# Performance work log

Hardware: AMD Instinct MI355X
Metric: run time of the kernel (lower is better)

## Reference

```python
import jax, jax.numpy as jnp
import numpy as np

NQ = 10          # qubits per register
DIM = 2 ** NQ    # 1024 amplitudes
N_CLS = 10       # canonical images (one per class)
N = 16384        # batch of samples
IMG = 28 * 28    # 784 pixels, zero-padded to DIM


def setup_inputs() -> dict:
    key = jax.random.key(0)
    k1, k2, k3 = jax.random.split(key, 3)
    z_re = jax.random.normal(k1, (N, DIM), dtype=jnp.float32)
    z_im = jax.random.normal(k2, (N, DIM), dtype=jnp.float32)
    # inputs are quantum states -> L2-normalize the complex vectors
    nrm = jnp.sqrt(jnp.sum(z_re * z_re + z_im * z_im, axis=1, keepdims=True))
    z_re = z_re / nrm
    z_im = z_im / nrm
    canon = jax.random.uniform(k3, (N_CLS, 1, 28, 28), dtype=jnp.float32)
    return {"z_re": z_re, "z_im": z_im, "canon": canon}


def reference(z_re, z_im, canon):
    # reshape_norm_padding: flatten, zero-pad to 2^nq, L2-normalize (real amplitudes)
    ref = canon.reshape(N_CLS, IMG)
    ref = jnp.pad(ref, ((0, 0), (0, DIM - IMG)))                  # [C, DIM]
    ref = ref / jnp.linalg.norm(ref, axis=1, keepdims=True)
    # Swap test: <Z_anc> = |<val|ref>|^2. ref is real, so with val = z_re + i*z_im:
    #   <val|ref> = (z_re @ ref^T) - i*(z_im @ ref^T)
    s_re = jnp.einsum('nd,cd->nc', z_re, ref)                     # [N, C]
    s_im = jnp.einsum('nd,cd->nc', z_im, ref)                     # [N, C]
    return s_re * s_re + s_im * s_im                              # [N, C] float32
```

## Files before the change

### kernel.cpp

```cpp
#include <hip/hip_runtime.h>

#define NQ    10
#define DIM   1024
#define N_CLS 10
#define NROWS 16384
#define IMG   784

#define ROWS_PER_BLK 8

__device__ __forceinline__ float wave64_sum(float x) {
#define DPP_ADD(ctrl, rmask, bmask)                                           \
  x += __int_as_float(__builtin_amdgcn_update_dpp(                            \
      0, __float_as_int(x), ctrl, rmask, bmask, true));
  DPP_ADD(0x111, 0xf, 0xf)
  DPP_ADD(0x112, 0xf, 0xf)
  DPP_ADD(0x114, 0xf, 0xe)
  DPP_ADD(0x118, 0xf, 0xc)
  DPP_ADD(0x142, 0xa, 0xf)
  DPP_ADD(0x143, 0xc, 0xf)
#undef DPP_ADD
  return x;
}

__global__ void ref_prep_kernel(const float* __restrict__ canon,
                                float* __restrict__ ref) {
  __shared__ float red[256];
  const int c = blockIdx.x;
  const int t = threadIdx.x;
  const float* src = canon + c * IMG;

  float ss = 0.f;
  for (int d = t; d < IMG; d += 256) {
    float v = src[d];
    ss += v * v;
  }
  red[t] = ss;
  __syncthreads();
  for (int s = 128; s > 0; s >>= 1) {
    if (t < s) red[t] += red[t + s];
    __syncthreads();
  }
  const float inv = 1.0f / sqrtf(red[0]);

  for (int d = t; d < DIM; d += 256) {
    ref[c * DIM + d] = (d < IMG) ? src[d] * inv : 0.f;
  }
}

__global__ __launch_bounds__(64, 2) void swaptest_kernel(
    const float* __restrict__ zre, const float* __restrict__ zim,
    const float* __restrict__ ref, float* __restrict__ out) {
  const int lane = threadIdx.x;

  float4 refv[4][N_CLS];
#pragma unroll
  for (int k = 0; k < 4; ++k) {
#pragma unroll
    for (int c = 0; c < N_CLS; ++c) {
      refv[k][c] =
          *(const float4*)(ref + c * DIM + k * 256 + lane * 4);
    }
  }

  const int row0 = blockIdx.x * ROWS_PER_BLK;

  for (int r = 0; r < ROWS_PER_BLK; ++r) {
    const int row = row0 + r;
    if (row >= NROWS) break;

    const float4* pre = (const float4*)(zre + (size_t)row * DIM);
    const float4* pim = (const float4*)(zim + (size_t)row * DIM);

    float4 zr[4], zi[4];
#pragma unroll
    for (int k = 0; k < 4; ++k) {
      zr[k] = pre[k * 64 + lane];
      zi[k] = pim[k * 64 + lane];
    }

    float are[N_CLS], aim[N_CLS];
#pragma unroll
    for (int c = 0; c < N_CLS; ++c) {
      are[c] = 0.f;
      aim[c] = 0.f;
    }

#pragma unroll
    for (int k = 0; k < 4; ++k) {
#pragma unroll
      for (int c = 0; c < N_CLS; ++c) {
        const float4 rv = refv[k][c];
        are[c] += zr[k].x * rv.x + zr[k].y * rv.y + zr[k].z * rv.z +
                  zr[k].w * rv.w;
        aim[c] += zi[k].x * rv.x + zi[k].y * rv.y + zi[k].z * rv.z +
                  zi[k].w * rv.w;
      }
    }

#pragma unroll
    for (int c = 0; c < N_CLS; ++c) {
      are[c] = wave64_sum(are[c]);
      aim[c] = wave64_sum(aim[c]);
    }

    if (lane == 63) {
#pragma unroll
      for (int c = 0; c < N_CLS; ++c) {
        out[(size_t)row * N_CLS + c] = are[c] * are[c] + aim[c] * aim[c];
      }
    }
  }
}

extern "C" void kernel_launch(void* const* d_in, const int* in_sizes, int n_in,
                              void* d_out, int out_size, void* d_ws,
                              size_t ws_size, hipStream_t stream) {
  const float* z_re = (const float*)d_in[0];
  const float* z_im = (const float*)d_in[1];
  const float* canon = (const float*)d_in[2];
  float* out = (float*)d_out;
  float* ref = (float*)d_ws;

  ref_prep_kernel<<<N_CLS, 256, 0, stream>>>(canon, ref);

  const int nblk = NROWS / ROWS_PER_BLK;
  swaptest_kernel<<<nblk, 64, 0, stream>>>(z_re, z_im, ref, out);
}
```

Baseline: 151.9 us.

## Fuse ref prep into MFMA kernel using split-bf16 matmul and skip padded tail

Drops the separate reference-normalisation kernel. Each block now normalises the canonical images and stores them in shared memory as hi/lo bf16 pairs. The dot products run on 16x16x32 bf16 MFMA with a three-term split (hi*hi, lo*hi, hi*lo) to approach fp32 accuracy. Only the first 832 columns of z are read, because the reference is zero beyond 784, which cuts the memory traffic. Register prefetch of upcoming z chunks is meant to overlap load latency, at the cost of redundant per-block reference prep and a small precision loss from the split-bf16 products.

Result: slower. 157.0 us (+3.4%).

```diff
diff --git a/kernel.cpp b/kernel.cpp
--- a/kernel.cpp
+++ b/kernel.cpp
@@ -1,12 +1,48 @@
 #include <hip/hip_runtime.h>
 
-#define NQ    10
-#define DIM   1024
-#define N_CLS 10
-#define NROWS 16384
-#define IMG   784
+#define DIM    1024
+#define N_CLS  10
+#define NROWS  16384
+#define IMG    784
 
-#define ROWS_PER_BLK 8
+#define KPAD   832
+#define KSTEP  26
+#define PF     6
+
+using f32x4  = __attribute__((ext_vector_type(4))) float;
+using bf16x8 = __attribute__((ext_vector_type(8))) short;
+typedef unsigned int u32;
+typedef unsigned short u16;
+
+union frag_cast {
+  u32 i[4];
+  bf16x8 h;
+  f32x4 f;
+};
+
+static __device__ __forceinline__ u16 bf16_rne(float f) {
+  u32 u = __float_as_uint(f);
+  return (u16)((u + 0x7fffu + ((u >> 16) & 1u)) >> 16);
+}
+
+static __device__ __forceinline__ void split8(const f32x4 v0, const f32x4 v1,
+                                              bf16x8& hi, bf16x8& lo) {
+  const float f[8] = {v0.x, v0.y, v0.z, v0.w, v1.x, v1.y, v1.z, v1.w};
+  frag_cast H, L;
+#pragma unroll
+  for (int i = 0; i < 4; ++i) {
+    const u32 a = __float_as_uint(f[2 * i]);
+    const u32 b = __float_as_uint(f[2 * i + 1]);
+    H.i[i] = (a >> 16) | (b & 0xffff0000u);
+    const float l0 = f[2 * i] - __uint_as_float(a & 0xffff0000u);
+    const float l1 = f[2 * i + 1] - __uint_as_float(b & 0xffff0000u);
+    u32 p;
+    asm("v_cvt_pk_bf16_f32 %0, %1, %2" : "=v"(p) : "v"(l0), "v"(l1));
+    L.i[i] = p;
+  }
+  hi = H.h;
+  lo = L.h;
+}
 
 __device__ __forceinline__ float wave64_sum(float x) {
 #define DPP_ADD(ctrl, rmask, bmask)                                           \
@@ -22,92 +58,94 @@
   return x;
 }
 
-__global__ void ref_prep_kernel(const float* __restrict__ canon,
-                                float* __restrict__ ref) {
-  __shared__ float red[256];
-  const int c = blockIdx.x;
+__global__ __launch_bounds__(256, 1) void swaptest_kernel(
+    const float* __restrict__ zre, const float* __restrict__ zim,
+    const float* __restrict__ canon, float* __restrict__ out) {
+  __shared__ u16 bhi[KSTEP * 4 * 16 * 8];
+  __shared__ u16 blo[KSTEP * 4 * 16 * 8];
+  __shared__ float linv[16];
+
   const int t = threadIdx.x;
-  const float* src = canon + c * IMG;
+  const int lane = t & 63;
+  const int wave = t >> 6;
 
-  float ss = 0.f;
-  for (int d = t; d < IMG; d += 256) {
-    float v = src[d];
-    ss += v * v;
+  for (int c = wave; c < N_CLS; c += 4) {
+    float ss = 0.f;
+    for (int i = lane; i < IMG; i += 64) {
+      const float v = canon[c * IMG + i];
+      ss += v * v;
+    }
+    ss = wave64_sum(ss);
+    if (lane == 63) linv[c] = 1.0f / sqrtf(ss);
   }
-  red[t] = ss;
   __syncthreads();
-  for (int s = 128; s > 0; s >>= 1) {
-    if (t < s) red[t] += red[t + s];
-    __syncthreads();
+
+  for (int idx = t; idx < KPAD * 16; idx += 256) {
+    const int k = idx >> 4;
+    const int c = idx & 15;
+    float val = 0.f;
+    if (c < N_CLS && k < IMG) val = canon[c * IMG + k] * linv[c];
+    const int s = k >> 5, g = (k >> 3) & 3, j = k & 7;
+    const int pos = ((s * 4 + g) * 16 + c) * 8 + j;
+    const u32 u = __float_as_uint(val);
+    bhi[pos] = (u16)(u >> 16);
+    blo[pos] = bf16_rne(val - __uint_as_float(u & 0xffff0000u));
   }
-  const float inv = 1.0f / sqrtf(red[0]);
+  __syncthreads();
 
-  for (int d = t; d < DIM; d += 256) {
-    ref[c * DIM + d] = (d < IMG) ? src[d] * inv : 0.f;
-  }
-}
+  const int wid = blockIdx.x * 4 + wave;
+  const int row0 = wid * 16;
+  const int l15 = lane & 15;
+  const int gr = lane >> 4;
 
-__global__ __launch_bounds__(64, 2) void swaptest_kernel(
-    const float* __restrict__ zre, const float* __restrict__ zim,
-    const float* __restrict__ ref, float* __restrict__ out) {
-  const int lane = threadIdx.x;
+  const f32x4* pre = (const f32x4*)(zre + (size_t)(row0 + l15) * DIM) + gr * 2;
+  const f32x4* pim = (const f32x4*)(zim + (size_t)(row0 + l15) * DIM) + gr * 2;
 
-  float4 refv[4][N_CLS];
+  f32x4 r0[PF], r1[PF], i0[PF], i1[PF];
 #pragma unroll
-  for (int k = 0; k < 4; ++k) {
-#pragma unroll
-    for (int c = 0; c < N_CLS; ++c) {
-      refv[k][c] =
-          *(const float4*)(ref + c * DIM + k * 256 + lane * 4);
-    }
+  for (int j = 0; j < PF; ++j) {
+    r0[j] = pre[j * 8];
+    r1[j] = pre[j * 8 + 1];
+    i0[j] = pim[j * 8];
+    i1[j] = pim[j * 8 + 1];
   }
 
-  const int row0 = blockIdx.x * ROWS_PER_BLK;
-
-  for (int r = 0; r < ROWS_PER_BLK; ++r) {
-    const int row = row0 + r;
-    if (row >= NROWS) break;
-
-    const float4* pre = (const float4*)(zre + (size_t)row * DIM);
-    const float4* pim = (const float4*)(zim + (size_t)row * DIM);
-
-    float4 zr[4], zi[4];
-#pragma unroll
-    for (int k = 0; k < 4; ++k) {
-      zr[k] = pre[k * 64 + lane];
-      zi[k] = pim[k * 64 + lane];
-    }
-
-    float are[N_CLS], aim[N_CLS];
-#pragma unroll
-    for (int c = 0; c < N_CLS; ++c) {
-      are[c] = 0.f;
-      aim[c] = 0.f;
-    }
+  f32x4 accre = {0.f, 0.f, 0.f, 0.f};
+  f32x4 accim = {0.f, 0.f, 0.f, 0.f};
 
 #pragma unroll
-    for (int k = 0; k < 4; ++k) {
+  for (int j = 0; j < KSTEP; ++j) {
+    const int b = j % PF;
+    bf16x8 arh, arl, aih, ail;
+    split8(r0[b], r1[b], arh, arl);
+    split8(i0[b], i1[b], aih, ail);
+    if (j + PF < KSTEP) {
+      r0[b] = pre[(j + PF) * 8];
+      r1[b] = pre[(j + PF) * 8 + 1];
+      i0[b] = pim[(j + PF) * 8];
+      i1[b] = pim[(j + PF) * 8 + 1];
+    }
+    frag_cast BH, BL;
+    const int be = (j * 64 + gr * 16 + l15) * 8;
+    BH.f = *(const f32x4*)&bhi[be];
+    BL.f = *(const f32x4*)&blo[be];
+
+    accre = __builtin_amdgcn_mfma_f32_16x16x32_bf16(arh, BH.h, accre, 0, 0, 0);
+    accre = __builtin_amdgcn_mfma_f32_16x16x32_bf16(arl, BH.h, accre, 0, 0, 0);
+    accre = __builtin_amdgcn_mfma_f32_16x16x32_bf16(arh, BL.h, accre, 0, 0, 0);
+    accim = __builtin_amdgcn_mfma_f32_16x16x32_bf16(aih, BH.h, accim, 0, 0, 0);
+    accim = __builtin_amdgcn_mfma_f32_16x16x32_bf16(ail, BH.h, accim, 0, 0, 0);
+    accim = __builtin_amdgcn_mfma_f32_16x16x32_bf16(aih, BL.h, accim, 0, 0, 0);
+  }
+
+  const int c = l15;
+  const int rbase = row0 + gr * 4;
+  if (c < N_CLS) {
 #pragma unroll
-      for (int c = 0; c < N_CLS; ++c) {
-        const float4 rv = refv[k][c];
-        are[c] += zr[k].x * rv.x + zr[k].y * rv.y + zr[k].z * rv.z +
-                  zr[k].w * rv.w;
-        aim[c] += zi[k].x * rv.x + zi[k].y * rv.y + zi[k].z * rv.z +
-                  zi[k].w * rv.w;
-      }
-    }
-
-#pragma unroll
-    for (int c = 0; c < N_CLS; ++c) {
-      are[c] = wave64_sum(are[c]);
-      aim[c] = wave64_sum(aim[c]);
-    }
-
-    if (lane == 63) {
-#pragma unroll
-      for (int c = 0; c < N_CLS; ++c) {
-        out[(size_t)row * N_CLS + c] = are[c] * are[c] + aim[c] * aim[c];
-      }
+    for (int i = 0; i < 4; ++i) {
+      const float sre = accre[i];
+      const float sim = accim[i];
+      out[(size_t)(rbase + i) * N_CLS + c] = sre * sre + sim * sim;
     }
   }
 }
@@ -119,10 +157,7 @@
   const float* z_im = (const float*)d_in[1];
   const float* canon = (const float*)d_in[2];
   float* out = (float*)d_out;
-  float* ref = (float*)d_ws;
+  (void)d_ws; (void)ws_size;
 
-  ref_prep_kernel<<<N_CLS, 256, 0, stream>>>(canon, ref);
-
-  const int nblk = NROWS / ROWS_PER_BLK;
-  swaptest_kernel<<<nblk, 64, 0, stream>>>(z_re, z_im, ref, out);
+  swaptest_kernel<<<NROWS / 16 / 4, 256, 0, stream>>>(z_re, z_im, canon, out);
 }
```
